# Kernel optimization log

Hardware: AMD Instinct MI355X
Metric: run time of the kernel (lower is better)

Reference implementation:

```python
import jax, jax.numpy as jnp
import numpy as np
from jax import lax

IMG = 512            # image H = W
FH = FW = 32         # feature map spatial size
A = 9                # anchors per location (3 sizes x 3 ratios)
N = FH * FW * A      # total anchors = 9216
IOU_THR = 0.7
MIN_SCORE = 0.5
MIN_SIZE = 1e-3


def make_anchors():
    """Anchors in centroid format (cx, cy, w, h), ordered (H, W, A)."""
    stride = IMG / FH
    sizes = np.array([32.0, 64.0, 128.0])
    ratios = np.array([0.5, 1.0, 2.0])
    ws = (sizes[:, None] / np.sqrt(ratios)[None, :]).reshape(-1)  # (A,)
    hs = (sizes[:, None] * np.sqrt(ratios)[None, :]).reshape(-1)  # (A,)
    cx = (np.arange(FW) + 0.5) * stride
    cy = (np.arange(FH) + 0.5) * stride
    CX = np.broadcast_to(cx[None, :, None], (FH, FW, A))
    CY = np.broadcast_to(cy[:, None, None], (FH, FW, A))
    Wg = np.broadcast_to(ws[None, None, :], (FH, FW, A))
    Hg = np.broadcast_to(hs[None, None, :], (FH, FW, A))
    anc = np.stack([CX, CY, Wg, Hg], axis=-1).reshape(-1, 4)
    return jnp.asarray(anc, dtype=jnp.float32)


def pairwise_iou(b):
    # b: (N,4) corners x1,y1,x2,y2
    x1, y1, x2, y2 = b[:, 0], b[:, 1], b[:, 2], b[:, 3]
    area = (x2 - x1) * (y2 - y1)
    ix1 = jnp.maximum(x1[:, None], x1[None, :])
    iy1 = jnp.maximum(y1[:, None], y1[None, :])
    ix2 = jnp.minimum(x2[:, None], x2[None, :])
    iy2 = jnp.minimum(y2[:, None], y2[None, :])
    inter = jnp.maximum(ix2 - ix1, 0.0) * jnp.maximum(iy2 - iy1, 0.0)
    union = area[:, None] + area[None, :] - inter
    return inter / jnp.maximum(union, 1e-9)


def nms_keep(boxes, scores, valid):
    """Greedy NMS. Returns bool keep mask of shape (N,). Index decisions only."""
    s = jnp.where(valid, scores, -jnp.inf)
    order = jnp.argsort(-s)
    b = boxes[order]
    v = valid[order]
    ious = pairwise_iou(b)  # (N, N)
    idx = jnp.arange(N)

    def body(i, supp):
        keep_i = (~supp[i]) & v[i]
        return supp | (keep_i & (ious[i] > IOU_THR) & (idx > i))

    supp = lax.fori_loop(0, N, body, jnp.zeros(N, dtype=bool))
    keep_sorted = (~supp) & v
    return jnp.zeros(N, dtype=bool).at[order].set(keep_sorted)


def setup_inputs() -> dict:
    key = jax.random.key(0)
    ks = jax.random.split(key, 4)
    return {
        "feature_map": jax.random.normal(ks[0], (1, 256, FH, FW), jnp.float32),
        "conv1_w": jax.random.normal(ks[1], (512, 256, 3, 3), jnp.float32) * 0.02,
        "conv1_b": jnp.zeros((512,), jnp.float32),
        "conv2_w": jax.random.normal(ks[2], (A, 512), jnp.float32) * 0.01,
        "conv2_b": jnp.zeros((A,), jnp.float32),
        "conv3_w": jax.random.normal(ks[3], (4 * A, 512), jnp.float32) * 0.01,
        "conv3_b": jnp.zeros((4 * A,), jnp.float32),
    }


def reference(feature_map, conv1_w, conv1_b, conv2_w, conv2_b, conv3_w, conv3_b):
    anchors = make_anchors()  # (N,4) cx,cy,w,h

    # --- conv backbone head ---
    h = lax.conv_general_dilated(
        feature_map, conv1_w, (1, 1), "SAME",
        dimension_numbers=("NCHW", "OIHW", "NCHW"))
    h = jax.nn.relu(h + conv1_b[None, :, None, None])  # (1,512,H,W)

    scores = jax.nn.sigmoid(
        jnp.einsum("bchw,ac->bahw", h, conv2_w) + conv2_b[None, :, None, None])
    scores = scores.transpose(0, 2, 3, 1).reshape(-1)  # (N,) ordered (H,W,A)

    off = jnp.einsum("bchw,oc->bohw", h, conv3_w) + conv3_b[None, :, None, None]
    off = off.reshape(1, A, 4, FH, FW).transpose(0, 3, 4, 1, 2).reshape(-1, 4)

    acx, acy, aw, ah = anchors[:, 0], anchors[:, 1], anchors[:, 2], anchors[:, 3]
    cx = acx + off[:, 0] * aw
    cy = acy + off[:, 1] * ah
    bw = aw * jnp.exp(off[:, 2])
    bh = ah * jnp.exp(off[:, 3])
    boxes = jnp.stack([cx - bw / 2, cy - bh / 2, cx + bw / 2, cy + bh / 2], axis=1)

    # --- clip to image ---
    lo = jnp.array([0.0, 0.0, 0.0, 0.0], jnp.float32)
    hi = jnp.array([IMG, IMG, IMG, IMG], jnp.float32)
    boxes = jnp.clip(boxes, lo, hi)

    # --- remove small boxes + score threshold (as a mask, jit-safe) ---
    valid = ((boxes[:, 2] - boxes[:, 0]) >= MIN_SIZE) \
          & ((boxes[:, 3] - boxes[:, 1]) >= MIN_SIZE) \
          & (scores >= MIN_SCORE)

    # --- NMS (selection is index-based; no gradient through the decision) ---
    keep = nms_keep(lax.stop_gradient(boxes), lax.stop_gradient(scores), valid)

    out = jnp.concatenate(
        [boxes * keep[:, None].astype(boxes.dtype),
         (scores * keep.astype(scores.dtype))[:, None]], axis=1)  # (N,5)
    return out
```

## Files before the change

kernel.cpp:

```cpp
#include <hip/hip_runtime.h>
#include <math.h>

#define FHW   32
#define NA    9
#define NBOX  9216
#define C1    256
#define C2    512
#define KTOT  2304
#define KS    8
#define KCH   (KTOT / KS)
#define CAP   64

struct AnchorWH { float w[NA]; float h[NA]; };

#define FP_OFF    0u
#define WT_OFF    1183744u
#define HP_OFF    5902336u
#define BOX_OFF   22679552u
#define SC_OFF    22827008u
#define VL_OFF    22863872u
#define DEG_OFF   22900736u
#define ADJ_OFF   22937600u
#define KEEP_OFF  24117248u
#define NV_OFF    24154112u

__global__ __launch_bounds__(256) void k_prep(const float* __restrict__ fin,
                                              float* __restrict__ Fp,
                                              unsigned int* __restrict__ deg,
                                              unsigned int* __restrict__ nv) {
    int idx = blockIdx.x * 256 + threadIdx.x;
    if (idx < 256 * 34 * 34) {
        int c   = idx / 1156;
        int rem = idx - c * 1156;
        int yy  = rem / 34;
        int xx  = rem - yy * 34;
        float v = 0.f;
        if (yy >= 1 && yy <= 32 && xx >= 1 && xx <= 32)
            v = fin[c * 1024 + (yy - 1) * 32 + (xx - 1)];
        Fp[idx] = v;
    }
    if (idx < NBOX) deg[idx] = 0u;
    if (idx == 0)   *nv = 0u;
}

__global__ __launch_bounds__(256) void k_tr(const float* __restrict__ w1,
                                            float* __restrict__ Wt) {
    __shared__ float tile[32][33];
    int k0  = blockIdx.x * 32;
    int oc0 = blockIdx.y * 32;
    int t   = threadIdx.x;
    int r0 = t >> 5, c = t & 31;
    #pragma unroll
    for (int i = 0; i < 4; ++i) {
        int r = r0 + 8 * i;
        tile[r][c] = w1[(oc0 + r) * KTOT + k0 + c];
    }
    __syncthreads();
    #pragma unroll
    for (int i = 0; i < 4; ++i) {
        int kk = r0 + 8 * i;
        Wt[(k0 + kk) * C2 + oc0 + c] = tile[c][kk];
    }
}

__global__ __launch_bounds__(256) void k_gemm(const float* __restrict__ Fp,
                                              const float* __restrict__ Wt,
                                              float* __restrict__ hp) {
    const int p0  = blockIdx.x * 128;
    const int oc0 = blockIdx.y * 128;
    const int ks  = blockIdx.z;
    const int k0b = ks * KCH;
    const int t   = threadIdx.x;
    const int ty  = t >> 4, tx = t & 15;

    __shared__ float As[16][128];
    __shared__ float Bs[16][128];

    float acc[8][8];
    #pragma unroll
    for (int r = 0; r < 8; ++r)
        #pragma unroll
        for (int c = 0; c < 8; ++c) acc[r][c] = 0.f;

    for (int kt = 0; kt < KCH; kt += 16) {
        #pragma unroll
        for (int i = 0; i < 8; ++i) {
            int e  = t + 256 * i;
            int kk = e >> 7, pp = e & 127;
            int k  = k0b + kt + kk;
            int c  = k / 9;
            int kap = k - c * 9;
            int dy = kap / 3;
            int dx = kap - dy * 3;
            int p  = p0 + pp;
            int y  = p >> 5, x = p & 31;
            As[kk][pp] = Fp[(c * 34 + y + dy) * 34 + x + dx];
        }
        #pragma unroll
        for (int i = 0; i < 8; ++i) {
            int e  = t + 256 * i;
            int kk = e >> 7, j = e & 127;
            Bs[kk][j] = Wt[(k0b + kt + kk) * C2 + oc0 + j];
        }
        __syncthreads();
        #pragma unroll
        for (int kk = 0; kk < 16; ++kk) {
            float a[8], b[8];
            *(float4*)&a[0] = *(const float4*)&As[kk][ty * 8];
            *(float4*)&a[4] = *(const float4*)&As[kk][ty * 8 + 4];
            *(float4*)&b[0] = *(const float4*)&Bs[kk][tx * 8];
            *(float4*)&b[4] = *(const float4*)&Bs[kk][tx * 8 + 4];
            #pragma unroll
            for (int r = 0; r < 8; ++r)
                #pragma unroll
                for (int c = 0; c < 8; ++c) acc[r][c] += a[r] * b[c];
        }
        __syncthreads();
    }
    #pragma unroll
    for (int r = 0; r < 8; ++r) {
        int p = p0 + ty * 8 + r;
        float* dst = hp + ((ks * 1024 + p) * C2 + oc0 + tx * 8);
        *(float4*)dst       = *(float4*)&acc[r][0];
        *(float4*)(dst + 4) = *(float4*)&acc[r][4];
    }
}

__global__ __launch_bounds__(256) void k_heads(const float* __restrict__ hp,
                                               const float* __restrict__ b1,
                                               const float* __restrict__ w2,
                                               const float* __restrict__ b2,
                                               const float* __restrict__ w3,
                                               const float* __restrict__ b3,
                                               float* __restrict__ boxes,
                                               float* __restrict__ scoresG,
                                               unsigned int* __restrict__ nv,
                                               unsigned int* __restrict__ vlist,
                                               AnchorWH awh) {
    const int p = blockIdx.x;
    const int t = threadIdx.x;
    __shared__ float hrow[C2];
    __shared__ float arr[45];

    #pragma unroll
    for (int i = 0; i < 2; ++i) {
        int c = t + 256 * i;
        float s = b1[c];
        #pragma unroll
        for (int ks = 0; ks < KS; ++ks) s += hp[(ks * 1024 + p) * C2 + c];
        hrow[c] = fmaxf(s, 0.f);
    }
    __syncthreads();

    const int w = t >> 6, lane = t & 63;
    float h8[8];
    #pragma unroll
    for (int i = 0; i < 8; ++i) h8[i] = hrow[lane + 64 * i];

    for (int j = w; j < 45; j += 4) {
        const float* wp = (j < 9) ? (w2 + j * C2) : (w3 + (j - 9) * C2);
        float s = 0.f;
        #pragma unroll
        for (int i = 0; i < 8; ++i) s += h8[i] * wp[lane + 64 * i];
        #pragma unroll
        for (int d = 1; d < 64; d <<= 1) s += __shfl_xor(s, d, 64);
        if (lane == 0) arr[j] = s;
    }
    __syncthreads();

    if (t < NA) {
        int a = t;
        float logit = arr[a] + b2[a];
        float score = 1.f / (1.f + expf(-logit));
        float o0 = arr[9 + a * 4 + 0] + b3[a * 4 + 0];
        float o1 = arr[9 + a * 4 + 1] + b3[a * 4 + 1];
        float o2 = arr[9 + a * 4 + 2] + b3[a * 4 + 2];
        float o3 = arr[9 + a * 4 + 3] + b3[a * 4 + 3];
        int y = p >> 5, x = p & 31;
        float ax = (x + 0.5f) * 16.f, ay = (y + 0.5f) * 16.f;
        float aw = awh.w[a], ah = awh.h[a];
        float cx = ax + o0 * aw;
        float cy = ay + o1 * ah;
        float bw = aw * expf(o2);
        float bh = ah * expf(o3);
        float x1 = fminf(fmaxf(cx - bw * 0.5f, 0.f), 512.f);
        float y1 = fminf(fmaxf(cy - bh * 0.5f, 0.f), 512.f);
        float x2 = fminf(fmaxf(cx + bw * 0.5f, 0.f), 512.f);
        float y2 = fminf(fmaxf(cy + bh * 0.5f, 0.f), 512.f);
        int n = p * 9 + a;
        float4 bx4; bx4.x = x1; bx4.y = y1; bx4.z = x2; bx4.w = y2;
        ((float4*)boxes)[n] = bx4;
        scoresG[n] = score;
        bool valid = (x2 - x1 >= 0.001f) && (y2 - y1 >= 0.001f) && (score >= 0.5f);
        if (valid) {
            unsigned int ci = atomicAdd(nv, 1u);
            vlist[ci] = (unsigned int)n;
        }
    }
}

__global__ __launch_bounds__(256) void k_adj(const unsigned int* __restrict__ nvp,
                                             const unsigned int* __restrict__ vlist,
                                             const float* __restrict__ boxes,
                                             const float* __restrict__ scoresG,
                                             unsigned int* __restrict__ deg,
                                             unsigned short* __restrict__ adj) {
    const int Nv = (int)*nvp;
    int b = blockIdx.x;
    int tv = (int)(sqrtf(2.f * b + 0.25f) - 0.5f);
    while ((tv + 1) * (tv + 2) / 2 <= b) tv++;
    while (tv * (tv + 1) / 2 > b) tv--;
    int tu = b - tv * (tv + 1) / 2;
    if (tv * 128 >= Nv) return;

    __shared__ float4 ub[128], vb[128];
    __shared__ float  us[128], vs[128];
    __shared__ int    uo[128], vo[128];
    int t = threadIdx.x;
    if (t < 128) {
        int gi = tu * 128 + t;
        if (gi < Nv) { int n = (int)vlist[gi]; ub[t] = ((const float4*)boxes)[n]; us[t] = scoresG[n]; uo[t] = n; }
        else us[t] = -1.f;
    } else {
        int tt = t - 128;
        int gj = tv * 128 + tt;
        if (gj < Nv) { int n = (int)vlist[gj]; vb[tt] = ((const float4*)boxes)[n]; vs[tt] = scoresG[n]; vo[tt] = n; }
        else vs[tt] = -1.f;
    }
    __syncthreads();

    for (int s = 0; s < 64; ++s) {
        int q  = t + 256 * s;
        int i  = q >> 7, jj = q & 127;
        if (tu == tv && i >= jj) continue;
        float su = us[i], sv = vs[jj];
        if (su < 0.f || sv < 0.f) continue;
        float4 bu = ub[i], bv = vb[jj];
        float au = (bu.z - bu.x) * (bu.w - bu.y);
        float av = (bv.z - bv.x) * (bv.w - bv.y);
        float ix1 = fmaxf(bu.x, bv.x), iy1 = fmaxf(bu.y, bv.y);
        float ix2 = fminf(bu.z, bv.z), iy2 = fminf(bu.w, bv.w);
        float inter = fmaxf(ix2 - ix1, 0.f) * fmaxf(iy2 - iy1, 0.f);
        float uni = au + av - inter;
        float iou = inter / fmaxf(uni, 1e-9f);
        if (iou > 0.7f) {
            int gi = tu * 128 + i, gj = tv * 128 + jj;
            bool uHigh = (su > sv) || (su == sv && uo[i] < vo[jj]);
            int lower = uHigh ? gj : gi;
            int upper = uHigh ? gi : gj;
            unsigned int slot = atomicAdd(&deg[lower], 1u);
            if (slot < CAP) adj[lower * CAP + slot] = (unsigned short)upper;
        }
    }
}

__global__ __launch_bounds__(1024) void k_peel(const unsigned int* __restrict__ nvp,
                                               const unsigned int* __restrict__ vlist,
                                               const unsigned int* __restrict__ deg,
                                               const unsigned short* __restrict__ adj,
                                               unsigned int* __restrict__ keep) {
    __shared__ unsigned char st[NBOX];
    __shared__ int changed;
    const int t = threadIdx.x;
    const int Nv = (int)*nvp;
    for (int n = t; n < NBOX; n += 1024) keep[n] = 0u;
    for (int i = t; i < Nv; i += 1024) st[i] = 0;
    __syncthreads();

    for (int round = 0; round < 512; ++round) {
        if (t == 0) changed = 0;
        __syncthreads();
        bool any = false;
        for (int i = t; i < Nv; i += 1024) {
            if (st[i] == 0) {
                int d = (int)deg[i]; if (d > CAP) d = CAP;
                bool kseen = false, useen = false;
                for (int s = 0; s < d; ++s) {
                    unsigned char v = st[adj[i * CAP + s]];
                    kseen |= (v == 1);
                    useen |= (v == 0);
                }
                if (kseen)      { st[i] = 2; any = true; }
                else if (!useen){ st[i] = 1; any = true; }
            }
        }
        if (any) changed = 1;
        __syncthreads();
        int c = changed;
        __syncthreads();
        if (!c) break;
    }
    for (int i = t; i < Nv; i += 1024)
        if (st[i] == 1) keep[vlist[i]] = 1u;
}

__global__ __launch_bounds__(256) void k_out(const float* __restrict__ boxes,
                                             const float* __restrict__ scoresG,
                                             const unsigned int* __restrict__ keep,
                                             float* __restrict__ out) {
    int n = blockIdx.x * 256 + threadIdx.x;
    if (n >= NBOX) return;
    float4 b = ((const float4*)boxes)[n];
    bool k = keep[n] != 0u;
    out[n * 5 + 0] = k ? b.x : 0.f;
    out[n * 5 + 1] = k ? b.y : 0.f;
    out[n * 5 + 2] = k ? b.z : 0.f;
    out[n * 5 + 3] = k ? b.w : 0.f;
    out[n * 5 + 4] = k ? scoresG[n] : 0.f;
}

extern "C" void kernel_launch(void* const* d_in, const int* in_sizes, int n_in,
                              void* d_out, int out_size, void* d_ws, size_t ws_size,
                              hipStream_t stream) {
    const float* fin = (const float*)d_in[0];
    const float* w1  = (const float*)d_in[1];
    const float* b1  = (const float*)d_in[2];
    const float* w2  = (const float*)d_in[3];
    const float* b2  = (const float*)d_in[4];
    const float* w3  = (const float*)d_in[5];
    const float* b3  = (const float*)d_in[6];
    float* out = (float*)d_out;

    char* ws = (char*)d_ws;
    float*          Fp    = (float*)(ws + FP_OFF);
    float*          Wt    = (float*)(ws + WT_OFF);
    float*          hp    = (float*)(ws + HP_OFF);
    float*          boxes = (float*)(ws + BOX_OFF);
    float*          sc    = (float*)(ws + SC_OFF);
    unsigned int*   vlist = (unsigned int*)(ws + VL_OFF);
    unsigned int*   deg   = (unsigned int*)(ws + DEG_OFF);
    unsigned short* adj   = (unsigned short*)(ws + ADJ_OFF);
    unsigned int*   keep  = (unsigned int*)(ws + KEEP_OFF);
    unsigned int*   nv    = (unsigned int*)(ws + NV_OFF);

    AnchorWH awh;
    {
        const double sizes[3]  = {32.0, 64.0, 128.0};
        const double ratios[3] = {0.5, 1.0, 2.0};
        for (int si = 0; si < 3; ++si)
            for (int ri = 0; ri < 3; ++ri) {
                awh.w[si * 3 + ri] = (float)(sizes[si] / sqrt(ratios[ri]));
                awh.h[si * 3 + ri] = (float)(sizes[si] * sqrt(ratios[ri]));
            }
    }

    k_prep<<<dim3((256 * 34 * 34 + 255) / 256), 256, 0, stream>>>(fin, Fp, deg, nv);
    k_tr<<<dim3(72, 16), 256, 0, stream>>>(w1, Wt);
    k_gemm<<<dim3(8, 4, KS), 256, 0, stream>>>(Fp, Wt, hp);
    k_heads<<<dim3(1024), 256, 0, stream>>>(hp, b1, w2, b2, w3, b3, boxes, sc, nv, vlist, awh);
    k_adj<<<dim3(72 * 73 / 2), 256, 0, stream>>>(nv, vlist, boxes, sc, deg, adj);
    k_peel<<<dim3(1), 1024, 0, stream>>>(nv, vlist, deg, adj, keep);
    k_out<<<dim3((NBOX + 255) / 256), 256, 0, stream>>>(boxes, sc, keep, out);
}
```

Baseline: 204.1 us.

## Merge weight transpose into prep kernel and retile GEMM to 64x64 blocks

The weight transpose is folded into the padding/prep kernel as extra blocks, removing one launch. The conv GEMM is retiled from 128x128 tiles with 256 threads to 64x64 tiles with 64 threads, giving 1024 blocks instead of 256 so more CUs are busy. B-tile loads become float4 and the im2col gather is restructured to one pixel per thread. Smaller tiles lower data reuse per block and raise the total global traffic.

```diff
diff --git a/kernel.cpp b/kernel.cpp
--- a/kernel.cpp
+++ b/kernel.cpp
@@ -27,54 +27,58 @@
 __global__ __launch_bounds__(256) void k_prep(const float* __restrict__ fin,
                                               float* __restrict__ Fp,
                                               unsigned int* __restrict__ deg,
-                                              unsigned int* __restrict__ nv) {
-    int idx = blockIdx.x * 256 + threadIdx.x;
-    if (idx < 256 * 34 * 34) {
-        int c   = idx / 1156;
-        int rem = idx - c * 1156;
-        int yy  = rem / 34;
-        int xx  = rem - yy * 34;
-        float v = 0.f;
-        if (yy >= 1 && yy <= 32 && xx >= 1 && xx <= 32)
-            v = fin[c * 1024 + (yy - 1) * 32 + (xx - 1)];
-        Fp[idx] = v;
-    }
-    if (idx < NBOX) deg[idx] = 0u;
-    if (idx == 0)   *nv = 0u;
-}
-
-__global__ __launch_bounds__(256) void k_tr(const float* __restrict__ w1,
-                                            float* __restrict__ Wt) {
-    __shared__ float tile[32][33];
-    int k0  = blockIdx.x * 32;
-    int oc0 = blockIdx.y * 32;
-    int t   = threadIdx.x;
-    int r0 = t >> 5, c = t & 31;
-    #pragma unroll
-    for (int i = 0; i < 4; ++i) {
-        int r = r0 + 8 * i;
-        tile[r][c] = w1[(oc0 + r) * KTOT + k0 + c];
-    }
-    __syncthreads();
-    #pragma unroll
-    for (int i = 0; i < 4; ++i) {
-        int kk = r0 + 8 * i;
-        Wt[(k0 + kk) * C2 + oc0 + c] = tile[c][kk];
-    }
-}
-
-__global__ __launch_bounds__(256) void k_gemm(const float* __restrict__ Fp,
-                                              const float* __restrict__ Wt,
-                                              float* __restrict__ hp) {
-    const int p0  = blockIdx.x * 128;
-    const int oc0 = blockIdx.y * 128;
-    const int ks  = blockIdx.z;
-    const int k0b = ks * KCH;
-    const int t   = threadIdx.x;
-    const int ty  = t >> 4, tx = t & 15;
-
-    __shared__ float As[16][128];
-    __shared__ float Bs[16][128];
+                                              unsigned int* __restrict__ nv,
+                                              const float* __restrict__ w1,
+                                              float* __restrict__ Wt) {
+    if (blockIdx.x < 1156) {
+        int idx = blockIdx.x * 256 + threadIdx.x;
+        if (idx < 256 * 34 * 34) {
+            int c   = idx / 1156;
+            int rem = idx - c * 1156;
+            int yy  = rem / 34;
+            int xx  = rem - yy * 34;
+            float v = 0.f;
+            if (yy >= 1 && yy <= 32 && xx >= 1 && xx <= 32)
+                v = fin[c * 1024 + (yy - 1) * 32 + (xx - 1)];
+            Fp[idx] = v;
+        }
+        if (idx < NBOX) deg[idx] = 0u;
+        if (idx == 0)   *nv = 0u;
+    } else {
+        __shared__ float tile[32][33];
+        int tb  = blockIdx.x - 1156;
+        int k0  = (tb % 72) * 32;
+        int oc0 = (tb / 72) * 32;
+        int t   = threadIdx.x;
+        int r0 = t >> 5, c = t & 31;
+        #pragma unroll
+        for (int i = 0; i < 4; ++i) {
+            int r = r0 + 8 * i;
+            tile[r][c] = w1[(oc0 + r) * KTOT + k0 + c];
+        }
+        __syncthreads();
+        #pragma unroll
+        for (int i = 0; i < 4; ++i) {
+            int kk = r0 + 8 * i;
+            Wt[(k0 + kk) * C2 + oc0 + c] = tile[c][kk];
+        }
+    }
+}
+
+__global__ __launch_bounds__(64, 1) void k_gemm(const float* __restrict__ Fp,
+                                                const float* __restrict__ Wt,
+                                                float* __restrict__ hp) {
+    const int id = blockIdx.x;
+    const int g  = id & 63, bx = id >> 6;
+    const int by = g >> 3, kz = g & 7;
+    const int p0  = bx * 64;
+    const int oc0 = by * 64;
+    const int k0b = kz * KCH;
+    const int t  = threadIdx.x;
+    const int r8 = t >> 3, c8 = t & 7;
+
+    __shared__ float As[16][64];
+    __shared__ float Bs[16][64];
 
     float acc[8][8];
     #pragma unroll
@@ -82,34 +86,33 @@
         #pragma unroll
         for (int c = 0; c < 8; ++c) acc[r][c] = 0.f;
 
+    const int p = p0 + t, y = p >> 5, x = p & 31;
+
     for (int kt = 0; kt < KCH; kt += 16) {
         #pragma unroll
-        for (int i = 0; i < 8; ++i) {
-            int e  = t + 256 * i;
-            int kk = e >> 7, pp = e & 127;
-            int k  = k0b + kt + kk;
-            int c  = k / 9;
+        for (int kk = 0; kk < 16; ++kk) {
+            int k   = k0b + kt + kk;
+            int c   = k / 9;
             int kap = k - c * 9;
-            int dy = kap / 3;
-            int dx = kap - dy * 3;
-            int p  = p0 + pp;
-            int y  = p >> 5, x = p & 31;
-            As[kk][pp] = Fp[(c * 34 + y + dy) * 34 + x + dx];
-        }
-        #pragma unroll
-        for (int i = 0; i < 8; ++i) {
-            int e  = t + 256 * i;
-            int kk = e >> 7, j = e & 127;
-            Bs[kk][j] = Wt[(k0b + kt + kk) * C2 + oc0 + j];
+            int dy  = kap / 3;
+            int dx  = kap - dy * 3;
+            As[kk][t] = Fp[(c * 34 + y + dy) * 34 + x + dx];
+        }
+        #pragma unroll
+        for (int i = 0; i < 4; ++i) {
+            int idx4 = t + 64 * i;
+            int kk = idx4 >> 4, c4 = idx4 & 15;
+            *(float4*)&Bs[kk][c4 * 4] =
+                *(const float4*)&Wt[(k0b + kt + kk) * C2 + oc0 + c4 * 4];
         }
         __syncthreads();
         #pragma unroll
         for (int kk = 0; kk < 16; ++kk) {
             float a[8], b[8];
-            *(float4*)&a[0] = *(const float4*)&As[kk][ty * 8];
-            *(float4*)&a[4] = *(const float4*)&As[kk][ty * 8 + 4];
-            *(float4*)&b[0] = *(const float4*)&Bs[kk][tx * 8];
-            *(float4*)&b[4] = *(const float4*)&Bs[kk][tx * 8 + 4];
+            *(float4*)&a[0] = *(const float4*)&As[kk][r8 * 4];
+            *(float4*)&a[4] = *(const float4*)&As[kk][r8 * 4 + 32];
+            *(float4*)&b[0] = *(const float4*)&Bs[kk][c8 * 4];
+            *(float4*)&b[4] = *(const float4*)&Bs[kk][c8 * 4 + 32];
             #pragma unroll
             for (int r = 0; r < 8; ++r)
                 #pragma unroll
@@ -119,10 +122,10 @@
     }
     #pragma unroll
     for (int r = 0; r < 8; ++r) {
-        int p = p0 + ty * 8 + r;
-        float* dst = hp + ((ks * 1024 + p) * C2 + oc0 + tx * 8);
-        *(float4*)dst       = *(float4*)&acc[r][0];
-        *(float4*)(dst + 4) = *(float4*)&acc[r][4];
+        int row = r8 * 4 + (r & 3) + 32 * (r >> 2);
+        float* dst = hp + ((kz * 1024 + p0 + row) * C2 + oc0 + c8 * 4);
+        *(float4*)dst        = *(float4*)&acc[r][0];
+        *(float4*)(dst + 32) = *(float4*)&acc[r][4];
     }
 }
 
@@ -344,9 +347,8 @@
             }
     }
 
-    k_prep<<<dim3((256 * 34 * 34 + 255) / 256), 256, 0, stream>>>(fin, Fp, deg, nv);
-    k_tr<<<dim3(72, 16), 256, 0, stream>>>(w1, Wt);
-    k_gemm<<<dim3(8, 4, KS), 256, 0, stream>>>(Fp, Wt, hp);
+    k_prep<<<dim3(1156 + 72 * 16), 256, 0, stream>>>(fin, Fp, deg, nv, w1, Wt);
+    k_gemm<<<dim3(1024), 64, 0, stream>>>(Fp, Wt, hp);
     k_heads<<<dim3(1024), 256, 0, stream>>>(hp, b1, w2, b2, w3, b3, boxes, sc, nv, vlist, awh);
     k_adj<<<dim3(72 * 73 / 2), 256, 0, stream>>>(nv, vlist, boxes, sc, deg, adj);
     k_peel<<<dim3(1), 1024, 0, stream>>>(nv, vlist, deg, adj, keep);
```

Measured after the change: 213.9 us. 1.05x slower.
